# Optimization experiments

Measured on AMD Instinct MI355X. Metric: run time of the kernel, lower is better.

## Reference

```python
import jax, jax.numpy as jnp
import numpy as np

B, S, HID = 2, 2048, 2816
NH, NKV, HD = 16, 8, 256
WINDOW = 1024
EPS = 1e-6
ROPE_THETA = 10000.0


def _rope_cos_sin(batch, seq, dim, theta):
    inv_freq = 1.0 / (theta ** (np.arange(0, dim, 2, dtype=np.float32) / dim))  # [dim/2]
    pos = np.arange(seq, dtype=np.float32)
    freqs = np.outer(pos, inv_freq)                 # [S, dim/2]
    emb = np.concatenate([freqs, freqs], axis=-1)   # [S, dim]
    cos = np.broadcast_to(np.cos(emb), (batch, seq, dim))
    sin = np.broadcast_to(np.sin(emb), (batch, seq, dim))
    return jnp.asarray(cos), jnp.asarray(sin)


def setup_inputs() -> dict:
    key = jax.random.key(0)
    ks = jax.random.split(key, 6)
    hidden_states = jax.random.normal(ks[0], (B, S, HID), dtype=jnp.float32)
    sc = 0.02
    Wq = jax.random.normal(ks[1], (NH * HD, HID), dtype=jnp.float32) * sc
    Wk = jax.random.normal(ks[2], (NKV * HD, HID), dtype=jnp.float32) * sc
    Wv = jax.random.normal(ks[3], (NKV * HD, HID), dtype=jnp.float32) * sc
    Wo = jax.random.normal(ks[4], (HID, NH * HD), dtype=jnp.float32) * sc
    q_norm_w = jnp.ones((HD,), dtype=jnp.float32) + 0.1 * jax.random.normal(ks[5], (HD,), dtype=jnp.float32)
    k_norm_w = jnp.ones((HD,), dtype=jnp.float32)
    cos, sin = _rope_cos_sin(B, S, HD, ROPE_THETA)
    return {"hidden_states": hidden_states, "Wq": Wq, "Wk": Wk, "Wv": Wv,
            "Wo": Wo, "q_norm_w": q_norm_w, "k_norm_w": k_norm_w,
            "cos": cos, "sin": sin}


def _rmsnorm(x, w):
    # HF Gemma4: effective weight, no +1 offset
    var = jnp.mean(jnp.square(x), axis=-1, keepdims=True)
    return x * jax.lax.rsqrt(var + EPS) * w


def _rotate_half(x):
    h = x.shape[-1] // 2
    return jnp.concatenate([-x[..., h:], x[..., :h]], axis=-1)


def reference(hidden_states, Wq, Wk, Wv, Wo, q_norm_w, k_norm_w, cos, sin):
    b, s, _ = hidden_states.shape
    q = (hidden_states @ Wq.T).reshape(b, s, NH, HD)
    k = (hidden_states @ Wk.T).reshape(b, s, NKV, HD)
    v = (hidden_states @ Wv.T).reshape(b, s, NKV, HD)
    q = _rmsnorm(q, q_norm_w)
    k = _rmsnorm(k, k_norm_w)
    v = _rmsnorm(v, jnp.ones((HD,), dtype=v.dtype))  # v_norm has no scale
    # RoPE with explicit cos/sin, unsqueeze at head dim (2)
    c = cos[:, :, None, :]
    sn = sin[:, :, None, :]
    q = q * c + _rotate_half(q) * sn
    k = k * c + _rotate_half(k) * sn
    # GQA: repeat kv heads to match query heads
    rep = NH // NKV
    k = jnp.repeat(k, rep, axis=2)  # [b,s,NH,HD]
    v = jnp.repeat(v, rep, axis=2)
    # scale=1.0 per torch_attention call (no 1/sqrt(d))
    scores = jnp.einsum('bqhd,bkhd->bhqk', q, k)
    i = jnp.arange(s)[:, None]
    j = jnp.arange(s)[None, :]
    mask = (j <= i) & (i - j < WINDOW)  # causal + sliding window
    scores = jnp.where(mask[None, None], scores, jnp.finfo(scores.dtype).min)
    attn = jax.nn.softmax(scores, axis=-1)
    out = jnp.einsum('bhqk,bkhd->bqhd', attn, v)  # [b,s,NH,HD]
    return out.reshape(b, s, NH * HD) @ Wo.T
```

## Files before the change

kernel.cpp:

```cpp
#include <hip/hip_runtime.h>
#include <math.h>

typedef unsigned short u16;
typedef __attribute__((ext_vector_type(8))) short short8;
typedef __attribute__((ext_vector_type(8))) _Float16 half8;
typedef __attribute__((ext_vector_type(4))) float floatx4;

#define NH 16
#define NKV 8
#define HD 256
#define SEQ 2048
#define BATCH 2
#define QD (NH * HD)
#define KVD (NKV * HD)
#define TOKS (BATCH * SEQ)
#define WINDOW 1024

__device__ __forceinline__ u16 f2h(float f) {
    _Float16 h = (_Float16)f;
    return __builtin_bit_cast(u16, h);
}
__device__ __forceinline__ float h2f(u16 u) {
    return (float)__builtin_bit_cast(_Float16, u);
}

__device__ __forceinline__ void gload16(const u16* g, u16* l) {
    __builtin_amdgcn_global_load_lds(
        (const __attribute__((address_space(1))) unsigned int*)g,
        (__attribute__((address_space(3))) unsigned int*)l,
        16, 0, 0);
}

__global__ __launch_bounds__(256) void f32_to_f16(const float* __restrict__ in,
                                                  u16* __restrict__ out, int n8) {
    const int i = blockIdx.x * 256 + threadIdx.x;
    if (i >= n8) return;
    const float4 a = *((const float4*)in + 2 * (size_t)i);
    const float4 b = *((const float4*)in + 2 * (size_t)i + 1);
    short8 r;
    r[0] = (short)f2h(a.x); r[1] = (short)f2h(a.y);
    r[2] = (short)f2h(a.z); r[3] = (short)f2h(a.w);
    r[4] = (short)f2h(b.x); r[5] = (short)f2h(b.y);
    r[6] = (short)f2h(b.z); r[7] = (short)f2h(b.w);
    *((short8*)out + i) = r;
}

template<int MODE>
__global__ __launch_bounds__(512, 4) void gemm_db(
        const u16* __restrict__ A, const u16* __restrict__ B,
        void* __restrict__ Cq, void* __restrict__ Ck, void* __restrict__ Cv,
        int N, int K, int ntn) {
    __shared__ u16 As[2 * 8192];
    __shared__ u16 Bs[2 * 4096];

    const int tid = threadIdx.x;
    const int wave = tid >> 6, lane = tid & 63;
    const int quad = lane >> 4, l16 = lane & 15;
    const int wr = wave >> 1, wc = wave & 1;

    const int nwg = (int)gridDim.x;
    const int wg0 = (int)blockIdx.x;
    const int wg = (wg0 & 7) * (nwg >> 3) + (wg0 >> 3);
    const int bm = (wg / ntn) * 256;
    const int bn = (wg % ntn) * 128;

    const int lrow = lane >> 2;
    const int lcol = (((lane & 3) ^ ((lane >> 3) & 3)) << 3);
    const u16* gA  = A + (size_t)(bm + wave * 32 + lrow) * K + lcol;
    const u16* gA2 = gA + (size_t)16 * K;
    const u16* gB  = B + (size_t)(bn + wave * 16 + lrow) * K + lcol;

    floatx4 acc[4][4];
#pragma unroll
    for (int i = 0; i < 4; ++i)
#pragma unroll
        for (int j = 0; j < 4; ++j) acc[i][j] = (floatx4){0.f, 0.f, 0.f, 0.f};

#define STG(tt, bb)                                                           \
    {                                                                         \
        const int ko_ = (tt) << 5;                                            \
        gload16(gA + ko_,  &As[(bb) * 8192 + wave * 1024]);                   \
        gload16(gA2 + ko_, &As[(bb) * 8192 + wave * 1024 + 512]);             \
        gload16(gB + ko_,  &Bs[(bb) * 4096 + wave * 512]);                    \
    }

    STG(0, 0);

    const int rdsw = ((quad ^ ((l16 >> 1) & 3)) << 3);
    const int aoff = (wr * 64 + l16) * 32 + rdsw;
    const int boff = (wc * 64 + l16) * 32 + rdsw;

    const int NT = K >> 5;
    for (int t = 0; t < NT; ++t) {
        const int cb = t & 1;
        if (t + 1 < NT) {
            STG(t + 1, cb ^ 1);
            asm volatile("s_waitcnt vmcnt(3)" ::: "memory");
        } else {
            asm volatile("s_waitcnt vmcnt(0)" ::: "memory");
        }
        __builtin_amdgcn_sched_barrier(0);
        __builtin_amdgcn_s_barrier();
        __builtin_amdgcn_sched_barrier(0);

        half8 aq[4], bq[4];
#pragma unroll
        for (int i = 0; i < 4; ++i)
            aq[i] = *(const half8*)(&As[cb * 8192 + aoff + i * 512]);
#pragma unroll
        for (int j = 0; j < 4; ++j)
            bq[j] = *(const half8*)(&Bs[cb * 4096 + boff + j * 512]);
#pragma unroll
        for (int i = 0; i < 4; ++i)
#pragma unroll
            for (int j = 0; j < 4; ++j)
                acc[i][j] = __builtin_amdgcn_mfma_f32_16x16x32_f16(aq[i], bq[j], acc[i][j], 0, 0, 0);

        __builtin_amdgcn_sched_barrier(0);
        __builtin_amdgcn_s_barrier();
        __builtin_amdgcn_sched_barrier(0);
    }
#undef STG

#pragma unroll
    for (int i = 0; i < 4; ++i) {
#pragma unroll
        for (int j = 0; j < 4; ++j) {
            const int row0 = bm + wr * 64 + i * 16 + quad * 4;
            const int col = bn + wc * 64 + j * 16 + l16;
#pragma unroll
            for (int r = 0; r < 4; ++r) {
                if constexpr (MODE == 1) {
                    ((float*)Cq)[(size_t)(row0 + r) * N + col] = acc[i][j][r];
                } else {
                    const u16 hv = f2h(acc[i][j][r]);
                    if (bn < 4096)
                        ((u16*)Cq)[(size_t)(row0 + r) * QD + col] = hv;
                    else if (bn < 6144)
                        ((u16*)Ck)[(size_t)(row0 + r) * KVD + (col - 4096)] = hv;
                    else
                        ((u16*)Cv)[(size_t)(col - 6144) * TOKS + row0 + r] = hv;
                }
            }
        }
    }
}

__global__ __launch_bounds__(256) void norm_rope_kernel(
        u16* __restrict__ Q, u16* __restrict__ K,
        const float* __restrict__ qw, const float* __restrict__ kw,
        const float* __restrict__ cosp, const float* __restrict__ sinp) {
    const int w = blockIdx.x * 4 + (threadIdx.x >> 6);
    const int lane = threadIdx.x & 63;
    const int row = w >> 5;
    const int sub = w & 31;
    if (sub >= 24) return;

    u16* ptr;
    const float* wt;
    if (sub < 16) { ptr = Q + (size_t)row * QD + sub * HD;         wt = qw; }
    else          { ptr = K + (size_t)row * KVD + (sub - 16) * HD; wt = kw; }

    const int d = lane * 4;
    uint2 raw = *(const uint2*)(ptr + d);
    float x[4];
    x[0] = h2f((u16)(raw.x & 0xffffu));
    x[1] = h2f((u16)(raw.x >> 16));
    x[2] = h2f((u16)(raw.y & 0xffffu));
    x[3] = h2f((u16)(raw.y >> 16));

    float ss = x[0] * x[0] + x[1] * x[1] + x[2] * x[2] + x[3] * x[3];
#pragma unroll
    for (int m = 1; m < 64; m <<= 1) ss += __shfl_xor(ss, m, 64);
    const float sc = rsqrtf(ss * (1.0f / 256.0f) + 1e-6f);

    float nrm[4];
#pragma unroll
    for (int i = 0; i < 4; ++i) nrm[i] = x[i] * sc * wt[d + i];

    const size_t cbase = (size_t)row * HD + d;
    const float sgn = (lane < 32) ? -1.0f : 1.0f;
    float out[4];
#pragma unroll
    for (int i = 0; i < 4; ++i) {
        float pn = __shfl_xor(nrm[i], 32, 64);
        float c = cosp[cbase + i];
        float s = sinp[cbase + i];
        out[i] = nrm[i] * c + sgn * pn * s;
    }

    uint2 o;
    o.x = (unsigned int)f2h(out[0]) | ((unsigned int)f2h(out[1]) << 16);
    o.y = (unsigned int)f2h(out[2]) | ((unsigned int)f2h(out[3]) << 16);
    *(uint2*)(ptr + d) = o;
}

__global__ __launch_bounds__(256) void vnorm_kernel(u16* __restrict__ Vt) {
    const int tok = blockIdx.x * 256 + threadIdx.x;
    const int kvh = blockIdx.y;
    u16* p = Vt + (size_t)kvh * HD * TOKS + tok;
    float ss = 0.f;
#pragma unroll 4
    for (int d = 0; d < HD; ++d) {
        float v = h2f(p[(size_t)d * TOKS]);
        ss += v * v;
    }
    const float sc = rsqrtf(ss * (1.0f / 256.0f) + 1e-6f);
#pragma unroll 4
    for (int d = 0; d < HD; ++d) {
        const size_t idx = (size_t)d * TOKS;
        p[idx] = f2h(h2f(p[idx]) * sc);
    }
}

#define QBLK 64
#define KVBLK 64

__global__ __launch_bounds__(256, 2) void attn_mfma(
        const u16* __restrict__ Q, const u16* __restrict__ K,
        const u16* __restrict__ Vt, u16* __restrict__ O) {
    __shared__ u16 Ks[64 * 256];
    __shared__ u16 Vs[256 * 64];
    __shared__ u16 Ps[4][16 * 72];

    const int tid = threadIdx.x;
    const int wave = tid >> 6, lane = tid & 63;
    const int quad = lane >> 4, l16 = lane & 15;
    const int q0 = blockIdx.x * QBLK;
    const int h = blockIdx.y, b = blockIdx.z;
    const int kvh = h >> 1;

    half8 qf[8];
    {
        const u16* qp = Q + (size_t)(b * SEQ + q0 + wave * 16 + l16) * QD + h * HD + quad * 8;
#pragma unroll
        for (int s = 0; s < 8; ++s) qf[s] = *(const half8*)(qp + s * 32);
    }

    float mrow[4], lrow[4];
#pragma unroll
    for (int r = 0; r < 4; ++r) { mrow[r] = -1e30f; lrow[r] = 0.f; }
    floatx4 o[16];
#pragma unroll
    for (int n = 0; n < 16; ++n) o[n] = (floatx4){0.f, 0.f, 0.f, 0.f};

    int lo = q0 - (WINDOW - 1);
    const int t0 = (lo > 0 ? lo : 0) >> 6;
    const int tq = q0 >> 6;

    const int kr2 = wave * 2 + (lane >> 5);
    const int kcb = (lane & 31) * 16;
    const int vr8 = wave * 8 + (lane >> 3);
    const int vcb = (lane & 7) * 16;

    for (int t = t0; t <= tq; ++t) {
        const int k0 = t * KVBLK;
        __syncthreads();
#pragma unroll
        for (int p = 0; p < 8; ++p) {
            const int row = p * 8 + kr2;
            const int scb = kcb ^ ((row & 7) << 4);
            const u16* g = K + (size_t)(b * SEQ + k0 + row) * KVD + kvh * HD + (scb >> 1);
            gload16(g, &Ks[p * 2048 + wave * 512]);
        }
#pragma unroll
        for (int p = 0; p < 8; ++p) {
            const int row = p * 32 + vr8;
            const int scb = vcb ^ ((row & 7) << 4);
            const u16* g = Vt + (size_t)(kvh * HD + row) * TOKS + b * SEQ + k0 + (scb >> 1);
            gload16(g, &Vs[p * 2048 + wave * 512]);
        }
        __syncthreads();

        floatx4 sf[4];
#pragma unroll
        for (int j = 0; j < 4; ++j) sf[j] = (floatx4){0.f, 0.f, 0.f, 0.f};
        __builtin_amdgcn_s_setprio(1);
#pragma unroll
        for (int s = 0; s < 8; ++s) {
#pragma unroll
            for (int j = 0; j < 4; ++j) {
                half8 bf = *(const half8*)(&Ks[(j * 16 + l16) * 256 +
                                               ((s * 32 + quad * 8) ^ ((l16 & 7) << 3))]);
                sf[j] = __builtin_amdgcn_mfma_f32_16x16x32_f16(qf[s], bf, sf[j], 0, 0, 0);
            }
        }
        __builtin_amdgcn_s_setprio(0);

        const bool needMask = (t == tq) || ((q0 + QBLK - 1) - k0 >= WINDOW);
        if (needMask) {
#pragma unroll
            for (int j = 0; j < 4; ++j) {
                const int kg = k0 + j * 16 + l16;
#pragma unroll
                for (int r = 0; r < 4; ++r) {
                    const int qg = q0 + wave * 16 + quad * 4 + r;
                    if (kg > qg || qg - kg >= WINDOW) sf[j][r] = -1e30f;
                }
            }
        }

#pragma unroll
        for (int r = 0; r < 4; ++r) {
            float mx = fmaxf(fmaxf(sf[0][r], sf[1][r]), fmaxf(sf[2][r], sf[3][r]));
            mx = fmaxf(mx, __shfl_xor(mx, 1, 64));
            mx = fmaxf(mx, __shfl_xor(mx, 2, 64));
            mx = fmaxf(mx, __shfl_xor(mx, 4, 64));
            mx = fmaxf(mx, __shfl_xor(mx, 8, 64));
            const float mnew = fmaxf(mrow[r], mx);
            const float rescale = __expf(mrow[r] - mnew);
            mrow[r] = mnew;
            float pv[4], ssum = 0.f;
#pragma unroll
            for (int j = 0; j < 4; ++j) {
                pv[j] = __expf(sf[j][r] - mnew);
                ssum += pv[j];
            }
            ssum += __shfl_xor(ssum, 1, 64);
            ssum += __shfl_xor(ssum, 2, 64);
            ssum += __shfl_xor(ssum, 4, 64);
            ssum += __shfl_xor(ssum, 8, 64);
            lrow[r] = lrow[r] * rescale + ssum;
#pragma unroll
            for (int n = 0; n < 16; ++n) o[n][r] *= rescale;
#pragma unroll
            for (int j = 0; j < 4; ++j)
                Ps[wave][(quad * 4 + r) * 72 + j * 16 + l16] = f2h(pv[j]);
        }

        __builtin_amdgcn_s_setprio(1);
#pragma unroll
        for (int s2 = 0; s2 < 2; ++s2) {
            half8 pa = *(const half8*)(&Ps[wave][l16 * 72 + s2 * 32 + quad * 8]);
#pragma unroll
            for (int n = 0; n < 16; ++n) {
                half8 vb = *(const half8*)(&Vs[(n * 16 + l16) * 64 +
                                               ((s2 * 32 + quad * 8) ^ ((l16 & 7) << 3))]);
                o[n] = __builtin_amdgcn_mfma_f32_16x16x32_f16(pa, vb, o[n], 0, 0, 0);
            }
        }
        __builtin_amdgcn_s_setprio(0);
    }

#pragma unroll
    for (int r = 0; r < 4; ++r) {
        const float inv = 1.0f / lrow[r];
        const size_t base = (size_t)(b * SEQ + q0 + wave * 16 + quad * 4 + r) * QD + h * HD + l16;
#pragma unroll
        for (int n = 0; n < 16; ++n)
            O[base + n * 16] = f2h(o[n][r] * inv);
    }
}

extern "C" void kernel_launch(void* const* d_in, const int* in_sizes, int n_in,
                              void* d_out, int out_size, void* d_ws, size_t ws_size,
                              hipStream_t stream) {
    const float* X    = (const float*)d_in[0];
    const float* Wq   = (const float*)d_in[1];
    const float* Wk   = (const float*)d_in[2];
    const float* Wv   = (const float*)d_in[3];
    const float* Wo   = (const float*)d_in[4];
    const float* qw   = (const float*)d_in[5];
    const float* kw   = (const float*)d_in[6];
    const float* cosp = (const float*)d_in[7];
    const float* sinp = (const float*)d_in[8];

    char* ws = (char*)d_ws;
    u16* Qb  = (u16*)(ws);
    u16* Kb  = (u16*)(ws + (size_t)33554432);
    u16* Vt  = (u16*)(ws + (size_t)50331648);
    u16* Xh  = (u16*)(ws + (size_t)67108864);
    u16* Ob  = (u16*)(ws + (size_t)67108864);
    u16* Woh = (u16*)(ws);

    u16* Wqkv = (u16*)d_out;

    const dim3 blk(256);
    f32_to_f16<<<dim3(5632), blk, 0, stream>>>(X,  Xh, 11534336 / 8);
    f32_to_f16<<<dim3(5632), blk, 0, stream>>>(Wq, Wqkv, 11534336 / 8);
    f32_to_f16<<<dim3(2816), blk, 0, stream>>>(Wk, Wqkv + (size_t)4096 * 2816, 5767168 / 8);
    f32_to_f16<<<dim3(2816), blk, 0, stream>>>(Wv, Wqkv + (size_t)6144 * 2816, 5767168 / 8);
    gemm_db<0><<<dim3(1024), dim3(512), 0, stream>>>(Xh, Wqkv, Qb, Kb, Vt, 8192, 2816, 64);
    norm_rope_kernel<<<dim3((BATCH * SEQ * 32) / 4), blk, 0, stream>>>(Qb, Kb, qw, kw, cosp, sinp);
    vnorm_kernel<<<dim3(TOKS / 256, NKV), blk, 0, stream>>>(Vt);
    attn_mfma<<<dim3(SEQ / QBLK, NH, BATCH), blk, 0, stream>>>(Qb, Kb, Vt, Ob);
    f32_to_f16<<<dim3(5632), blk, 0, stream>>>(Wo, Woh, 11534336 / 8);
    gemm_db<1><<<dim3(352), dim3(512), 0, stream>>>(Ob, Woh, d_out, nullptr, nullptr, 2816, 4096, 22);
}
```

Measured before the change: 731.9 us.

## Enlarge GEMM tile to 256x256 with four-stage LDS prefetch pipeline

The projection GEMM tile grows from 256x128 to 256x256, so each wave computes an 8x4 block of MFMA fragments. The LDS ring buffer goes from two to four stages, with loads issued three tiles ahead and graded vmcnt waits. The MFMA loop is also wrapped in raised wave priority. This raises arithmetic intensity and hides global-load latency. In exchange it doubles LDS use, adds register pressure (occupancy bound drops to 2) and halves the grid, and the output GEMM's 176 blocks underfill the GPU's compute units.

New measurement: 808.3 us. +10.4%, slower.

```diff
diff --git a/kernel.cpp b/kernel.cpp
--- a/kernel.cpp
+++ b/kernel.cpp
@@ -46,56 +46,65 @@
 }
 
 template<int MODE>
-__global__ __launch_bounds__(512, 4) void gemm_db(
+__global__ __launch_bounds__(512, 2) void gemm_r4(
         const u16* __restrict__ A, const u16* __restrict__ B,
         void* __restrict__ Cq, void* __restrict__ Ck, void* __restrict__ Cv,
         int N, int K, int ntn) {
-    __shared__ u16 As[2 * 8192];
-    __shared__ u16 Bs[2 * 4096];
+    __shared__ u16 As[4 * 8192];
+    __shared__ u16 Bs[4 * 8192];
 
     const int tid = threadIdx.x;
     const int wave = tid >> 6, lane = tid & 63;
     const int quad = lane >> 4, l16 = lane & 15;
-    const int wr = wave >> 1, wc = wave & 1;
+    const int wr = wave >> 2, wc = wave & 3;
 
     const int nwg = (int)gridDim.x;
     const int wg0 = (int)blockIdx.x;
     const int wg = (wg0 & 7) * (nwg >> 3) + (wg0 >> 3);
     const int bm = (wg / ntn) * 256;
-    const int bn = (wg % ntn) * 128;
+    const int bn = (wg % ntn) * 256;
 
     const int lrow = lane >> 2;
     const int lcol = (((lane & 3) ^ ((lane >> 3) & 3)) << 3);
     const u16* gA  = A + (size_t)(bm + wave * 32 + lrow) * K + lcol;
     const u16* gA2 = gA + (size_t)16 * K;
-    const u16* gB  = B + (size_t)(bn + wave * 16 + lrow) * K + lcol;
-
-    floatx4 acc[4][4];
-#pragma unroll
-    for (int i = 0; i < 4; ++i)
+    const u16* gB  = B + (size_t)(bn + wave * 32 + lrow) * K + lcol;
+    const u16* gB2 = gB + (size_t)16 * K;
+
+    floatx4 acc[8][4];
+#pragma unroll
+    for (int i = 0; i < 8; ++i)
 #pragma unroll
         for (int j = 0; j < 4; ++j) acc[i][j] = (floatx4){0.f, 0.f, 0.f, 0.f};
 
-#define STG(tt, bb)                                                           \
+#define STG(tt)                                                               \
     {                                                                         \
         const int ko_ = (tt) << 5;                                            \
-        gload16(gA + ko_,  &As[(bb) * 8192 + wave * 1024]);                   \
-        gload16(gA2 + ko_, &As[(bb) * 8192 + wave * 1024 + 512]);             \
-        gload16(gB + ko_,  &Bs[(bb) * 4096 + wave * 512]);                    \
-    }
-
-    STG(0, 0);
+        const int sl_ = ((tt) & 3) * 8192;                                    \
+        gload16(gA + ko_,  &As[sl_ + wave * 1024]);                           \
+        gload16(gA2 + ko_, &As[sl_ + wave * 1024 + 512]);                     \
+        gload16(gB + ko_,  &Bs[sl_ + wave * 1024]);                           \
+        gload16(gB2 + ko_, &Bs[sl_ + wave * 1024 + 512]);                     \
+    }
+
+    STG(0);
+    STG(1);
+    STG(2);
 
     const int rdsw = ((quad ^ ((l16 >> 1) & 3)) << 3);
-    const int aoff = (wr * 64 + l16) * 32 + rdsw;
+    const int aoff = (wr * 128 + l16) * 32 + rdsw;
     const int boff = (wc * 64 + l16) * 32 + rdsw;
 
     const int NT = K >> 5;
     for (int t = 0; t < NT; ++t) {
-        const int cb = t & 1;
-        if (t + 1 < NT) {
-            STG(t + 1, cb ^ 1);
-            asm volatile("s_waitcnt vmcnt(3)" ::: "memory");
+        const int sl = (t & 3) * 8192;
+        if (t + 3 < NT) {
+            STG(t + 3);
+            asm volatile("s_waitcnt vmcnt(12)" ::: "memory");
+        } else if (t + 2 < NT) {
+            asm volatile("s_waitcnt vmcnt(8)" ::: "memory");
+        } else if (t + 1 < NT) {
+            asm volatile("s_waitcnt vmcnt(4)" ::: "memory");
         } else {
             asm volatile("s_waitcnt vmcnt(0)" ::: "memory");
         }
@@ -103,18 +112,20 @@
         __builtin_amdgcn_s_barrier();
         __builtin_amdgcn_sched_barrier(0);
 
-        half8 aq[4], bq[4];
-#pragma unroll
-        for (int i = 0; i < 4; ++i)
-            aq[i] = *(const half8*)(&As[cb * 8192 + aoff + i * 512]);
+        half8 aq[8], bq[4];
 #pragma unroll
         for (int j = 0; j < 4; ++j)
-            bq[j] = *(const half8*)(&Bs[cb * 4096 + boff + j * 512]);
-#pragma unroll
-        for (int i = 0; i < 4; ++i)
+            bq[j] = *(const half8*)(&Bs[sl + boff + j * 512]);
+#pragma unroll
+        for (int i = 0; i < 8; ++i)
+            aq[i] = *(const half8*)(&As[sl + aoff + i * 512]);
+        __builtin_amdgcn_s_setprio(1);
+#pragma unroll
+        for (int i = 0; i < 8; ++i)
 #pragma unroll
             for (int j = 0; j < 4; ++j)
                 acc[i][j] = __builtin_amdgcn_mfma_f32_16x16x32_f16(aq[i], bq[j], acc[i][j], 0, 0, 0);
+        __builtin_amdgcn_s_setprio(0);
 
         __builtin_amdgcn_sched_barrier(0);
         __builtin_amdgcn_s_barrier();
@@ -123,10 +134,10 @@
 #undef STG
 
 #pragma unroll
-    for (int i = 0; i < 4; ++i) {
+    for (int i = 0; i < 8; ++i) {
 #pragma unroll
         for (int j = 0; j < 4; ++j) {
-            const int row0 = bm + wr * 64 + i * 16 + quad * 4;
+            const int row0 = bm + wr * 128 + i * 16 + quad * 4;
             const int col = bn + wc * 64 + j * 16 + l16;
 #pragma unroll
             for (int r = 0; r < 4; ++r) {
@@ -380,10 +391,10 @@
     f32_to_f16<<<dim3(5632), blk, 0, stream>>>(Wq, Wqkv, 11534336 / 8);
     f32_to_f16<<<dim3(2816), blk, 0, stream>>>(Wk, Wqkv + (size_t)4096 * 2816, 5767168 / 8);
     f32_to_f16<<<dim3(2816), blk, 0, stream>>>(Wv, Wqkv + (size_t)6144 * 2816, 5767168 / 8);
-    gemm_db<0><<<dim3(1024), dim3(512), 0, stream>>>(Xh, Wqkv, Qb, Kb, Vt, 8192, 2816, 64);
+    gemm_r4<0><<<dim3(512), dim3(512), 0, stream>>>(Xh, Wqkv, Qb, Kb, Vt, 8192, 2816, 32);
     norm_rope_kernel<<<dim3((BATCH * SEQ * 32) / 4), blk, 0, stream>>>(Qb, Kb, qw, kw, cosp, sinp);
     vnorm_kernel<<<dim3(TOKS / 256, NKV), blk, 0, stream>>>(Vt);
     attn_mfma<<<dim3(SEQ / QBLK, NH, BATCH), blk, 0, stream>>>(Qb, Kb, Vt, Ob);
     f32_to_f16<<<dim3(5632), blk, 0, stream>>>(Wo, Woh, 11534336 / 8);
-    gemm_db<1><<<dim3(352), dim3(512), 0, stream>>>(Ob, Woh, d_out, nullptr, nullptr, 2816, 4096, 22);
-}
+    gemm_r4<1><<<dim3(176), dim3(512), 0, stream>>>(Ob, Woh, d_out, nullptr, nullptr, 2816, 4096, 11);
+}
```
